# Kernel optimization log

Hardware: AMD Instinct MI355X
Metric: run time of the kernel (lower is better)

## Reference

```python
import jax, jax.numpy as jnp
import numpy as np

ALPHA = 0.95
GAMMA = 8.0
REFRACTORY_STEPS = 2.0
THETA_INC = 0.35
THETA_DECAY = 0.995

B, N, T = 16, 2048, 1000


def setup_inputs() -> dict:
    key = jax.random.key(0)
    u = jax.random.normal(key, (B, N, T), dtype=jnp.float32)
    theta_base = jnp.ones((1, N, 1), dtype=jnp.float32)
    return {"u": u, "theta_base": theta_base}


def surrogate_spike(x):
    # forward: Heaviside (x >= 0); surrogate grad handled in fwdbwd module
    return (x >= 0).astype(x.dtype)


def reference(u, theta_base):
    # u: [B, N, T]; theta_base: [1, N, 1]
    b, n, t = u.shape
    tb = theta_base[0, :, 0]  # [N], broadcasts over batch
    v0 = jnp.zeros((b, n), dtype=u.dtype)
    theta0 = jnp.broadcast_to(tb, (b, n)).astype(u.dtype)
    ref0 = jnp.zeros((b, n), dtype=u.dtype)

    def step(carry, u_t):
        v, theta_dyn, ref = carry
        ref_active = (ref > 0).astype(u_t.dtype)
        u_eff = u_t * (1.0 - ref_active)
        v = ALPHA * v + u_eff
        theta = theta_dyn  # adaptive_theta=True
        s = surrogate_spike(v - theta)
        v = v - s * theta  # soft reset (hard_reset=False)
        ref = jnp.maximum(ref - 1.0, 0.0)
        ref = jnp.where(s > 0, jnp.full_like(ref, REFRACTORY_STEPS), ref)
        theta_dyn = theta_dyn * THETA_DECAY + tb * (1.0 - THETA_DECAY) + THETA_INC * s
        return (v, theta_dyn, ref), (s, v)

    u_t_first = jnp.transpose(u, (2, 0, 1))  # [T, B, N]
    _, (spikes, v_hist) = jax.lax.scan(step, (v0, theta0, ref0), u_t_first)
    spikes = jnp.transpose(spikes, (1, 2, 0))  # [B, N, T]
    v_hist = jnp.transpose(v_hist, (1, 2, 0))
    return spikes, v_hist
```

## Files before the change

### kernel.cpp

```cpp
#include <hip/hip_runtime.h>


constexpr int B_ = 16;
constexpr int N_ = 2048;
constexpr int T_ = 1000;
constexpr int CH = 64;
constexpr int NCH = 16;
constexpr long NEUR = (long)B_ * N_;

#define LGKM0()                                                \
    do {                                                       \
        asm volatile("s_waitcnt lgkmcnt(0)" ::: "memory");     \
        __builtin_amdgcn_sched_barrier(0);                     \
    } while (0)

__device__ __forceinline__ void gload_lds16(const float* g, void* lds) {
    __builtin_amdgcn_global_load_lds(
        (const __attribute__((address_space(1))) void*)g,
        (__attribute__((address_space(3))) void*)lds, 16, 0, 0);
}

__global__ __launch_bounds__(192) void lif_pass1(
    const float* __restrict__ u,
    const float* __restrict__ theta_base,
    float* __restrict__ vhist,
    unsigned long long* __restrict__ wsbits)
{
    __shared__ float4 u_ring[3][64][16];
    __shared__ float4 v_lds[2][64][16];

    const int lane = threadIdx.x & 63;
    const int wid = threadIdx.x >> 6;
    const int blk0 = blockIdx.x * 64;

    if (wid == 1) {
        const float* ub = u + (size_t)blk0 * T_;
        const int rs = lane >> 4;
        const int sl = lane & 15;

        auto issue = [&](int c) {
            const int bq = c % 3;
            if (c < 15) {
                const int t0 = c * CH;
#pragma unroll
                for (int k = 0; k < 16; ++k) {
                    const int r = 4 * k + rs;
                    const float* g =
                        ub + (size_t)r * T_ + t0 + 4 * (sl ^ (r & 15));
                    gload_lds16(g, &u_ring[bq][4 * k][0]);
                }
            } else {
#pragma unroll
                for (int k = 0; k < 16; ++k) {
                    const int r = 4 * k + rs;
                    const int tf = sl ^ (r & 15);
                    if (tf < 10) {
                        const float* g = ub + (size_t)r * T_ + 960 + 4 * tf;
                        gload_lds16(g, &u_ring[bq][4 * k][0]);
                    }
                }
            }
        };

        issue(0);
        issue(1);
        asm volatile("s_waitcnt vmcnt(16)" ::: "memory");
        __builtin_amdgcn_sched_barrier(0);
        __builtin_amdgcn_s_barrier();
#pragma unroll 1
        for (int c = 0; c < NCH; ++c) {
            if (c + 2 < NCH) {
                issue(c + 2);
                asm volatile("s_waitcnt vmcnt(16)" ::: "memory");
            } else {
                asm volatile("s_waitcnt vmcnt(0)" ::: "memory");
            }
            __builtin_amdgcn_sched_barrier(0);
            __builtin_amdgcn_s_barrier();
            __builtin_amdgcn_sched_barrier(0);
        }
    } else if (wid == 0) {
        const float tb = theta_base[(blk0 + lane) & (N_ - 1)];
        const float c5 = __fmul_rn(tb, 0.005f);
        float v = 0.0f, theta = tb, ref = 0.0f;
        const int sw = lane & 15;

        __builtin_amdgcn_s_barrier();
#pragma unroll 1
        for (int c = 0; c < NCH; ++c) {
            const int bq = c % 3;
            const int pb = c & 1;
            float4 ubuf[16];
#pragma unroll
            for (int tf = 0; tf < 16; ++tf)
                ubuf[tf] = u_ring[bq][lane][tf ^ sw];
            unsigned blo = 0, bhi = 0;
#pragma unroll
            for (int tf = 0; tf < 16; ++tf) {
                const float uin[4] = {ubuf[tf].x, ubuf[tf].y,
                                      ubuf[tf].z, ubuf[tf].w};
                float vo[4];
#pragma unroll
                for (int k = 0; k < 4; ++k) {
                    const float ueff = (ref > 0.0f) ? 0.0f : uin[k];
                    v = __fadd_rn(__fmul_rn(0.95f, v), ueff);
                    const float d = __fsub_rn(v, theta);
                    const bool s = (d >= 0.0f);
                    v = s ? __fsub_rn(v, theta) : v;
                    ref = fmaxf(__fsub_rn(ref, 1.0f), 0.0f);
                    ref = s ? 2.0f : ref;
                    theta = __fadd_rn(__fmul_rn(theta, 0.995f), c5);
                    theta = s ? __fadd_rn(theta, 0.35f) : theta;

                    if (tf < 8) blo |= (s ? 1u : 0u) << (4 * tf + k);
                    else        bhi |= (s ? 1u : 0u) << (4 * (tf - 8) + k);
                    vo[k] = v;
                }
                v_lds[pb][lane][tf ^ sw] =
                    make_float4(vo[0], vo[1], vo[2], vo[3]);
            }
            wsbits[(size_t)c * NEUR + blk0 + lane] =
                ((unsigned long long)bhi << 32) | blo;
            LGKM0();
            __builtin_amdgcn_s_barrier();
        }
    } else {
        float* gv = vhist + (size_t)blk0 * T_;
        const int rs = lane >> 4;
        const int sl = lane & 15;

        __builtin_amdgcn_s_barrier();
#pragma unroll 1
        for (int c = 0; c < NCH; ++c) {
            if (c >= 1) {
                const int pc = c - 1;
                const int pb = pc & 1;
                const int t0 = pc * CH;
#pragma unroll
                for (int k = 0; k < 16; ++k) {
                    const int r = 4 * k + rs;
                    const float4 w = v_lds[pb][r][sl ^ (r & 15)];
                    *(float4*)(gv + (size_t)r * T_ + t0 + 4 * sl) = w;
                }
            }
            LGKM0();
            __builtin_amdgcn_s_barrier();
        }
#pragma unroll
        for (int k = 0; k < 16; ++k) {
            const int r = 4 * k + rs;
            if (sl < 10) {
                const float4 w = v_lds[1][r][sl ^ (r & 15)];
                *(float4*)(gv + (size_t)r * T_ + 960 + 4 * sl) = w;
            }
        }
    }
}

__global__ __launch_bounds__(256) void lif_expand(
    const unsigned* __restrict__ wsbits,
    float* __restrict__ spikes)
{
    const int tid = blockIdx.x * 256 + threadIdx.x;
    const int lane = tid & 63;
    const long wavei = tid >> 6;
    const long row = 2 * wavei + (lane >> 5);
    const int k = lane & 31;
    const int c = k >> 1;
    const int half = k & 1;

    const unsigned w = wsbits[(((size_t)c * NEUR + row) << 1) | half];
    const int t0 = 64 * c + 32 * half;
    float* gp = spikes + (size_t)row * T_ + t0;

#pragma unroll
    for (int j = 0; j < 8; ++j) {
        if (t0 + 4 * j < T_) {
            float4 f;
            f.x = ((w >> (4 * j + 0)) & 1u) ? 1.0f : 0.0f;
            f.y = ((w >> (4 * j + 1)) & 1u) ? 1.0f : 0.0f;
            f.z = ((w >> (4 * j + 2)) & 1u) ? 1.0f : 0.0f;
            f.w = ((w >> (4 * j + 3)) & 1u) ? 1.0f : 0.0f;
            *(float4*)(gp + 4 * j) = f;
        }
    }
}

extern "C" void kernel_launch(void* const* d_in, const int* in_sizes, int n_in,
                              void* d_out, int out_size, void* d_ws, size_t ws_size,
                              hipStream_t stream) {
    const float* u = (const float*)d_in[0];
    const float* theta_base = (const float*)d_in[1];
    float* out = (float*)d_out;
    float* spikes = out;
    float* vhist = out + (size_t)B_ * N_ * T_;
    unsigned long long* wsbits = (unsigned long long*)d_ws;

    lif_pass1<<<NEUR / 64, 192, 0, stream>>>(u, theta_base, vhist, wsbits);
    lif_expand<<<NEUR / 8, 256, 0, stream>>>((const unsigned*)wsbits, spikes);
}
```

Before: 122.4 us.

## Shrink pass1 blocks to 16 neurons per block to raise block count

Each pass1 block now handles 16 neurons instead of 64, so four times as many blocks are launched. Only 16 lanes of the compute wave run the recurrence, and the LDS rings and the load and store loops shrink to match. The compute lane now double-buffers its LDS reads in groups of four float4s, and launch bounds request 6 blocks per CU. The aim is better hiding of the serial recurrence latency across many more resident blocks, at the cost of leaving 48 of 64 compute lanes idle and doing more barrier overhead per neuron.

```diff
diff --git a/kernel.cpp b/kernel.cpp
--- a/kernel.cpp
+++ b/kernel.cpp
@@ -4,7 +4,9 @@
 constexpr int B_ = 16;
 constexpr int N_ = 2048;
 constexpr int T_ = 1000;
+constexpr int RPB = 16;
 constexpr int CH = 64;
+constexpr int NF4 = CH / 4;
 constexpr int NCH = 16;
 constexpr long NEUR = (long)B_ * N_;
 
@@ -20,18 +22,18 @@
         (__attribute__((address_space(3))) void*)lds, 16, 0, 0);
 }
 
-__global__ __launch_bounds__(192) void lif_pass1(
+__global__ __launch_bounds__(192, 6) void lif_pass1(
     const float* __restrict__ u,
     const float* __restrict__ theta_base,
     float* __restrict__ vhist,
     unsigned long long* __restrict__ wsbits)
 {
-    __shared__ float4 u_ring[3][64][16];
-    __shared__ float4 v_lds[2][64][16];
+    __shared__ float4 u_ring[3][RPB][NF4];
+    __shared__ float4 v_lds[2][RPB][NF4];
 
     const int lane = threadIdx.x & 63;
     const int wid = threadIdx.x >> 6;
-    const int blk0 = blockIdx.x * 64;
+    const int blk0 = blockIdx.x * RPB;
 
     if (wid == 1) {
         const float* ub = u + (size_t)blk0 * T_;
@@ -43,20 +45,20 @@
             if (c < 15) {
                 const int t0 = c * CH;
 #pragma unroll
-                for (int k = 0; k < 16; ++k) {
-                    const int r = 4 * k + rs;
+                for (int j = 0; j < 4; ++j) {
+                    const int r = 4 * j + rs;
                     const float* g =
                         ub + (size_t)r * T_ + t0 + 4 * (sl ^ (r & 15));
-                    gload_lds16(g, &u_ring[bq][4 * k][0]);
+                    gload_lds16(g, &u_ring[bq][4 * j][0]);
                 }
             } else {
 #pragma unroll
-                for (int k = 0; k < 16; ++k) {
-                    const int r = 4 * k + rs;
+                for (int j = 0; j < 4; ++j) {
+                    const int r = 4 * j + rs;
                     const int tf = sl ^ (r & 15);
                     if (tf < 10) {
                         const float* g = ub + (size_t)r * T_ + 960 + 4 * tf;
-                        gload_lds16(g, &u_ring[bq][4 * k][0]);
+                        gload_lds16(g, &u_ring[bq][4 * j][0]);
                     }
                 }
             }
@@ -64,14 +66,14 @@
 
         issue(0);
         issue(1);
-        asm volatile("s_waitcnt vmcnt(16)" ::: "memory");
+        asm volatile("s_waitcnt vmcnt(4)" ::: "memory");
         __builtin_amdgcn_sched_barrier(0);
         __builtin_amdgcn_s_barrier();
 #pragma unroll 1
         for (int c = 0; c < NCH; ++c) {
             if (c + 2 < NCH) {
                 issue(c + 2);
-                asm volatile("s_waitcnt vmcnt(16)" ::: "memory");
+                asm volatile("s_waitcnt vmcnt(4)" ::: "memory");
             } else {
                 asm volatile("s_waitcnt vmcnt(0)" ::: "memory");
             }
@@ -80,47 +82,67 @@
             __builtin_amdgcn_sched_barrier(0);
         }
     } else if (wid == 0) {
-        const float tb = theta_base[(blk0 + lane) & (N_ - 1)];
+        const float tb = theta_base[(blk0 + (lane & 15)) & (N_ - 1)];
         const float c5 = __fmul_rn(tb, 0.005f);
         float v = 0.0f, theta = tb, ref = 0.0f;
-        const int sw = lane & 15;
 
         __builtin_amdgcn_s_barrier();
 #pragma unroll 1
         for (int c = 0; c < NCH; ++c) {
             const int bq = c % 3;
             const int pb = c & 1;
-            float4 ubuf[16];
-#pragma unroll
-            for (int tf = 0; tf < 16; ++tf)
-                ubuf[tf] = u_ring[bq][lane][tf ^ sw];
-            unsigned blo = 0, bhi = 0;
-#pragma unroll
-            for (int tf = 0; tf < 16; ++tf) {
-                const float uin[4] = {ubuf[tf].x, ubuf[tf].y,
-                                      ubuf[tf].z, ubuf[tf].w};
-                float vo[4];
-#pragma unroll
-                for (int k = 0; k < 4; ++k) {
-                    const float ueff = (ref > 0.0f) ? 0.0f : uin[k];
-                    v = __fadd_rn(__fmul_rn(0.95f, v), ueff);
-                    const float d = __fsub_rn(v, theta);
-                    const bool s = (d >= 0.0f);
-                    v = s ? __fsub_rn(v, theta) : v;
-                    ref = fmaxf(__fsub_rn(ref, 1.0f), 0.0f);
-                    ref = s ? 2.0f : ref;
-                    theta = __fadd_rn(__fmul_rn(theta, 0.995f), c5);
-                    theta = s ? __fadd_rn(theta, 0.35f) : theta;
-
-                    if (tf < 8) blo |= (s ? 1u : 0u) << (4 * tf + k);
-                    else        bhi |= (s ? 1u : 0u) << (4 * (tf - 8) + k);
-                    vo[k] = v;
-                }
-                v_lds[pb][lane][tf ^ sw] =
-                    make_float4(vo[0], vo[1], vo[2], vo[3]);
-            }
-            wsbits[(size_t)c * NEUR + blk0 + lane] =
-                ((unsigned long long)bhi << 32) | blo;
+            if (lane < RPB) {
+                unsigned blo = 0, bhi = 0;
+                float4 ga[4], gb[4];
+#pragma unroll
+                for (int i = 0; i < 4; ++i)
+                    ga[i] = u_ring[bq][lane][(0 + i) ^ lane];
+
+                auto chain16 = [&](const float4 (&gr)[4], int gbase,
+                                   unsigned& bw) {
+#pragma unroll
+                    for (int i = 0; i < 4; ++i) {
+                        const int tf = gbase + i;
+                        const float uin[4] = {gr[i].x, gr[i].y,
+                                              gr[i].z, gr[i].w};
+                        float vo[4];
+#pragma unroll
+                        for (int k = 0; k < 4; ++k) {
+                            const float ueff = (ref > 0.0f) ? 0.0f : uin[k];
+                            v = __fadd_rn(__fmul_rn(0.95f, v), ueff);
+                            const float d = __fsub_rn(v, theta);
+                            const bool s = (d >= 0.0f);
+                            v = s ? __fsub_rn(v, theta) : v;
+                            ref = fmaxf(__fsub_rn(ref, 1.0f), 0.0f);
+                            ref = s ? 2.0f : ref;
+                            theta = __fadd_rn(__fmul_rn(theta, 0.995f), c5);
+                            theta = s ? __fadd_rn(theta, 0.35f) : theta;
+
+                            bw |= (s ? 1u : 0u) << (4 * ((tf & 7)) + k);
+                            vo[k] = v;
+                        }
+                        v_lds[pb][lane][tf ^ lane] =
+                            make_float4(vo[0], vo[1], vo[2], vo[3]);
+                    }
+                };
+
+#pragma unroll
+                for (int i = 0; i < 4; ++i)
+                    gb[i] = u_ring[bq][lane][(4 + i) ^ lane];
+                chain16(ga, 0, blo);
+#pragma unroll
+                for (int i = 0; i < 4; ++i)
+                    ga[i] = u_ring[bq][lane][(8 + i) ^ lane];
+                chain16(gb, 4, blo);
+#pragma unroll
+                for (int i = 0; i < 4; ++i)
+                    gb[i] = u_ring[bq][lane][(12 + i) ^ lane];
+                chain16(ga, 8, bhi);
+                chain16(gb, 12, bhi);
+
+                wsbits[(size_t)c * NEUR + blk0 + lane] =
+                    ((unsigned long long)bhi << 32) | blo;
+            }
             LGKM0();
             __builtin_amdgcn_s_barrier();
         }
@@ -137,8 +159,8 @@
                 const int pb = pc & 1;
                 const int t0 = pc * CH;
 #pragma unroll
-                for (int k = 0; k < 16; ++k) {
-                    const int r = 4 * k + rs;
+                for (int j = 0; j < 4; ++j) {
+                    const int r = 4 * j + rs;
                     const float4 w = v_lds[pb][r][sl ^ (r & 15)];
                     *(float4*)(gv + (size_t)r * T_ + t0 + 4 * sl) = w;
                 }
@@ -147,8 +169,8 @@
             __builtin_amdgcn_s_barrier();
         }
 #pragma unroll
-        for (int k = 0; k < 16; ++k) {
-            const int r = 4 * k + rs;
+        for (int j = 0; j < 4; ++j) {
+            const int r = 4 * j + rs;
             if (sl < 10) {
                 const float4 w = v_lds[1][r][sl ^ (r & 15)];
                 *(float4*)(gv + (size_t)r * T_ + 960 + 4 * sl) = w;
@@ -196,6 +218,8 @@
     float* vhist = out + (size_t)B_ * N_ * T_;
     unsigned long long* wsbits = (unsigned long long*)d_ws;
 
-    lif_pass1<<<NEUR / 64, 192, 0, stream>>>(u, theta_base, vhist, wsbits);
-    lif_expand<<<NEUR / 8, 256, 0, stream>>>((const unsigned*)wsbits, spikes);
-}
+    lif_pass1<<<(int)(NEUR / RPB), 192, 0, stream>>>(u, theta_base, vhist,
+                                                     wsbits);
+    lif_expand<<<(int)(NEUR / 8), 256, 0, stream>>>((const unsigned*)wsbits,
+                                                    spikes);
+}
```

Result: slower. 140.2 us (+14.5%).

## Replace warp-specialized LDS pipeline with single-wave register triple-buffering

Applied to the files above, without the earlier changes.

The pass-1 kernel no longer uses three specialized waves (loader, compute, storer) synchronised by barriers. A single 64-thread wave now loads each neuron's u chunk directly from global memory into registers, triple-buffered so the loads overlap the serial recurrence. It still writes v_hist through an LDS transpose for coalesced stores. This removes the barrier handshakes and async LDS loads, but each lane now reads a contiguous row, which coalesces poorly, and register pressure rises with 48 float4 buffers.

```diff
diff --git a/kernel.cpp b/kernel.cpp
--- a/kernel.cpp
+++ b/kernel.cpp
@@ -5,156 +5,116 @@
 constexpr int N_ = 2048;
 constexpr int T_ = 1000;
 constexpr int CH = 64;
-constexpr int NCH = 16;
 constexpr long NEUR = (long)B_ * N_;
 
-#define LGKM0()                                                \
-    do {                                                       \
-        asm volatile("s_waitcnt lgkmcnt(0)" ::: "memory");     \
-        __builtin_amdgcn_sched_barrier(0);                     \
-    } while (0)
-
-__device__ __forceinline__ void gload_lds16(const float* g, void* lds) {
-    __builtin_amdgcn_global_load_lds(
-        (const __attribute__((address_space(1))) void*)g,
-        (__attribute__((address_space(3))) void*)lds, 16, 0, 0);
-}
-
-__global__ __launch_bounds__(192) void lif_pass1(
+__global__ __launch_bounds__(64) void lif_pass1(
     const float* __restrict__ u,
     const float* __restrict__ theta_base,
     float* __restrict__ vhist,
     unsigned long long* __restrict__ wsbits)
 {
-    __shared__ float4 u_ring[3][64][16];
-    __shared__ float4 v_lds[2][64][16];
+    __shared__ float4 vt[2][64][16];
 
-    const int lane = threadIdx.x & 63;
-    const int wid = threadIdx.x >> 6;
+    const int lane = threadIdx.x;
     const int blk0 = blockIdx.x * 64;
+    const float tb = theta_base[(blk0 + lane) & (N_ - 1)];
+    const float c5 = __fmul_rn(tb, 0.005f);
+    float v = 0.0f, theta = tb, ref = 0.0f;
+    const float* up = u + (size_t)(blk0 + lane) * T_;
+    float* gv = vhist + (size_t)blk0 * T_;
+    const int sw = lane & 15;
+    const int rs = lane >> 4;
 
-    if (wid == 1) {
-        const float* ub = u + (size_t)blk0 * T_;
-        const int rs = lane >> 4;
-        const int sl = lane & 15;
+    float4 A[16], Bb[16], C[16];
 
-        auto issue = [&](int c) {
-            const int bq = c % 3;
-            if (c < 15) {
-                const int t0 = c * CH;
+    auto loadf = [&](float4 (&b)[16], int c) {
 #pragma unroll
-                for (int k = 0; k < 16; ++k) {
-                    const int r = 4 * k + rs;
-                    const float* g =
-                        ub + (size_t)r * T_ + t0 + 4 * (sl ^ (r & 15));
-                    gload_lds16(g, &u_ring[bq][4 * k][0]);
-                }
-            } else {
+        for (int i = 0; i < 16; ++i)
+            b[i] = *(const float4*)(up + CH * c + 4 * i);
+    };
+    auto loadt = [&](float4 (&b)[16]) {
 #pragma unroll
-                for (int k = 0; k < 16; ++k) {
-                    const int r = 4 * k + rs;
-                    const int tf = sl ^ (r & 15);
-                    if (tf < 10) {
-                        const float* g = ub + (size_t)r * T_ + 960 + 4 * tf;
-                        gload_lds16(g, &u_ring[bq][4 * k][0]);
-                    }
-                }
-            }
-        };
+        for (int i = 0; i < 10; ++i)
+            b[i] = *(const float4*)(up + 960 + 4 * i);
+    };
 
-        issue(0);
-        issue(1);
-        asm volatile("s_waitcnt vmcnt(16)" ::: "memory");
-        __builtin_amdgcn_sched_barrier(0);
-        __builtin_amdgcn_s_barrier();
-#pragma unroll 1
-        for (int c = 0; c < NCH; ++c) {
-            if (c + 2 < NCH) {
-                issue(c + 2);
-                asm volatile("s_waitcnt vmcnt(16)" ::: "memory");
-            } else {
-                asm volatile("s_waitcnt vmcnt(0)" ::: "memory");
-            }
-            __builtin_amdgcn_sched_barrier(0);
-            __builtin_amdgcn_s_barrier();
-            __builtin_amdgcn_sched_barrier(0);
+    auto step4 = [&](const float4 u4, unsigned& bw, int sh) -> float4 {
+        const float uin[4] = {u4.x, u4.y, u4.z, u4.w};
+        float vo[4];
+#pragma unroll
+        for (int k = 0; k < 4; ++k) {
+            const float ueff = (ref > 0.0f) ? 0.0f : uin[k];
+            v = __fadd_rn(__fmul_rn(0.95f, v), ueff);
+            const float d = __fsub_rn(v, theta);
+            const bool s = (d >= 0.0f);
+            v = s ? __fsub_rn(v, theta) : v;
+            ref = fmaxf(__fsub_rn(ref, 1.0f), 0.0f);
+            ref = s ? 2.0f : ref;
+            theta = __fadd_rn(__fmul_rn(theta, 0.995f), c5);
+            theta = s ? __fadd_rn(theta, 0.35f) : theta;
+
+            bw |= (s ? 1u : 0u) << (sh + k);
+            vo[k] = v;
         }
-    } else if (wid == 0) {
-        const float tb = theta_base[(blk0 + lane) & (N_ - 1)];
-        const float c5 = __fmul_rn(tb, 0.005f);
-        float v = 0.0f, theta = tb, ref = 0.0f;
-        const int sw = lane & 15;
+        return make_float4(vo[0], vo[1], vo[2], vo[3]);
+    };
 
-        __builtin_amdgcn_s_barrier();
-#pragma unroll 1
-        for (int c = 0; c < NCH; ++c) {
-            const int bq = c % 3;
-            const int pb = c & 1;
-            float4 ubuf[16];
+    auto do_chunk = [&](const float4 (&b)[16], int c) {
+        const int pb = c & 1;
+        unsigned blo = 0, bhi = 0;
 #pragma unroll
-            for (int tf = 0; tf < 16; ++tf)
-                ubuf[tf] = u_ring[bq][lane][tf ^ sw];
-            unsigned blo = 0, bhi = 0;
-#pragma unroll
-            for (int tf = 0; tf < 16; ++tf) {
-                const float uin[4] = {ubuf[tf].x, ubuf[tf].y,
-                                      ubuf[tf].z, ubuf[tf].w};
-                float vo[4];
-#pragma unroll
-                for (int k = 0; k < 4; ++k) {
-                    const float ueff = (ref > 0.0f) ? 0.0f : uin[k];
-                    v = __fadd_rn(__fmul_rn(0.95f, v), ueff);
-                    const float d = __fsub_rn(v, theta);
-                    const bool s = (d >= 0.0f);
-                    v = s ? __fsub_rn(v, theta) : v;
-                    ref = fmaxf(__fsub_rn(ref, 1.0f), 0.0f);
-                    ref = s ? 2.0f : ref;
-                    theta = __fadd_rn(__fmul_rn(theta, 0.995f), c5);
-                    theta = s ? __fadd_rn(theta, 0.35f) : theta;
-
-                    if (tf < 8) blo |= (s ? 1u : 0u) << (4 * tf + k);
-                    else        bhi |= (s ? 1u : 0u) << (4 * (tf - 8) + k);
-                    vo[k] = v;
-                }
-                v_lds[pb][lane][tf ^ sw] =
-                    make_float4(vo[0], vo[1], vo[2], vo[3]);
-            }
-            wsbits[(size_t)c * NEUR + blk0 + lane] =
-                ((unsigned long long)bhi << 32) | blo;
-            LGKM0();
-            __builtin_amdgcn_s_barrier();
+        for (int f = 0; f < 16; ++f) {
+            float4 v4 = (f < 8) ? step4(b[f], blo, 4 * f)
+                                : step4(b[f], bhi, 4 * (f - 8));
+            vt[pb][lane][f ^ sw] = v4;
         }
-    } else {
-        float* gv = vhist + (size_t)blk0 * T_;
-        const int rs = lane >> 4;
-        const int sl = lane & 15;
-
-        __builtin_amdgcn_s_barrier();
-#pragma unroll 1
-        for (int c = 0; c < NCH; ++c) {
-            if (c >= 1) {
-                const int pc = c - 1;
-                const int pb = pc & 1;
-                const int t0 = pc * CH;
-#pragma unroll
-                for (int k = 0; k < 16; ++k) {
-                    const int r = 4 * k + rs;
-                    const float4 w = v_lds[pb][r][sl ^ (r & 15)];
-                    *(float4*)(gv + (size_t)r * T_ + t0 + 4 * sl) = w;
-                }
-            }
-            LGKM0();
-            __builtin_amdgcn_s_barrier();
-        }
+        wsbits[(size_t)c * NEUR + blk0 + lane] =
+            ((unsigned long long)bhi << 32) | blo;
+        asm volatile("s_waitcnt lgkmcnt(0)" ::: "memory");
+        const int t0 = CH * c;
 #pragma unroll
         for (int k = 0; k < 16; ++k) {
             const int r = 4 * k + rs;
-            if (sl < 10) {
-                const float4 w = v_lds[1][r][sl ^ (r & 15)];
-                *(float4*)(gv + (size_t)r * T_ + 960 + 4 * sl) = w;
+            const float4 w = vt[pb][r][sw ^ (r & 15)];
+            *(float4*)(gv + (size_t)r * T_ + t0 + 4 * sw) = w;
+        }
+    };
+
+    auto do_tail = [&](const float4 (&b)[16]) {
+        const int pb = 1;
+        unsigned blo = 0, bhi = 0;
+#pragma unroll
+        for (int f = 0; f < 10; ++f) {
+            float4 v4 = (f < 8) ? step4(b[f], blo, 4 * f)
+                                : step4(b[f], bhi, 4 * (f - 8));
+            vt[pb][lane][f ^ sw] = v4;
+        }
+        wsbits[(size_t)15 * NEUR + blk0 + lane] =
+            ((unsigned long long)bhi << 32) | blo;
+        asm volatile("s_waitcnt lgkmcnt(0)" ::: "memory");
+#pragma unroll
+        for (int k = 0; k < 16; ++k) {
+            const int r = 4 * k + rs;
+            if (sw < 10) {
+                const float4 w = vt[pb][r][sw ^ (r & 15)];
+                *(float4*)(gv + (size_t)r * T_ + 960 + 4 * sw) = w;
             }
         }
+    };
+
+    loadf(A, 0);
+    loadf(Bb, 1);
+#pragma unroll 1
+    for (int g = 0; g < 5; ++g) {
+        loadf(C, 3 * g + 2);
+        do_chunk(A, 3 * g);
+        if (3 * g + 3 < 15) loadf(A, 3 * g + 3);
+        else                loadt(A);
+        do_chunk(Bb, 3 * g + 1);
+        if (3 * g + 4 < 15) loadf(Bb, 3 * g + 4);
+        do_chunk(C, 3 * g + 2);
     }
+    do_tail(A);
 }
 
 __global__ __launch_bounds__(256) void lif_expand(
@@ -193,9 +153,11 @@
     const float* theta_base = (const float*)d_in[1];
     float* out = (float*)d_out;
     float* spikes = out;
-    float* vhist = out + (size_t)B_ * N_ * T_;
+    float* vhist = out + (size_t)NEUR * T_;
     unsigned long long* wsbits = (unsigned long long*)d_ws;
 
-    lif_pass1<<<NEUR / 64, 192, 0, stream>>>(u, theta_base, vhist, wsbits);
-    lif_expand<<<NEUR / 8, 256, 0, stream>>>((const unsigned*)wsbits, spikes);
+    lif_pass1<<<(int)(NEUR / 64), 64, 0, stream>>>(u, theta_base, vhist,
+                                                   wsbits);
+    lif_expand<<<(int)(NEUR / 8), 256, 0, stream>>>((const unsigned*)wsbits,
+                                                    spikes);
 }
```

Result: slower. 128.5 us (+5.0%).
